# Performance work log

Measured on AMD Instinct MI355X. Metric: run time of the kernel, lower is better.

The kernel has to match this reference:

```python
import jax, jax.numpy as jnp
import numpy as np

EPS = 1e-5  # torch nn.LayerNorm default

def _ln(x, g, b):
    # LayerNorm over last dim with per-position affine params g, b (broadcastable)
    m = jnp.mean(x, axis=-1, keepdims=True)
    v = jnp.mean((x - m) ** 2, axis=-1, keepdims=True)
    return (x - m) * jax.lax.rsqrt(v + EPS) * g + b

def _mlp_ln(s, W1, b1, W2, b2, g, b):
    # Linear -> SiLU -> Linear -> LayerNorm
    h = jax.nn.silu(s @ W1 + b1) @ W2 + b2
    return _ln(h, g, b)

def setup_inputs() -> dict:
    key = jax.random.key(0)
    B, S, D = 4, 2048, 1024
    MEM, NOI, RES = 512, 64, 32
    ks = jax.random.split(key, 40)
    ki = iter(range(40))
    def nrm(shape, scale=0.02):
        return (jax.random.normal(ks[next(ki)], shape, jnp.float32) * scale)
    def gamma(shape):
        return jnp.ones(shape, jnp.float32) + nrm(shape)
    inp = {
        'x': jax.random.normal(ks[next(ki)], (B, S, D), jnp.float32),
        'pathway_ids': jax.random.randint(ks[next(ki)], (B, S), 0, 1000),
        'compartment_ids': jax.random.randint(ks[next(ki)], (B, S), 0, 5),
        'time_steps': jax.random.randint(ks[next(ki)], (B, S), 0, 5),
        'scale_type': jax.random.randint(ks[next(ki)], (B, S), 0, 3),
        'memory_state': jax.random.normal(ks[next(ki)], (B, MEM), jnp.float32),
        'noise_state': jax.random.normal(ks[next(ki)], (B, NOI), jnp.float32),
        'resource_state': jax.random.normal(ks[next(ki)], (B, RES), jnp.float32),
        # per-pathway / compartment / time / scale LayerNorm affine tables
        'pw_g': gamma((1000, D)), 'pw_b': nrm((1000, D)),
        'cp_g': gamma((5, D)), 'cp_b': nrm((5, D)),
        'tm_g': gamma((5, D)), 'tm_b': nrm((5, D)),
        'ms_g': gamma((3, D)), 'ms_b': nrm((3, D)),
        # memory / stochastic / resource MLP+LN stacks
        'mem_W1': nrm((MEM, D)), 'mem_b1': jnp.zeros((D,)), 'mem_W2': nrm((D, D)), 'mem_b2': jnp.zeros((D,)), 'mem_g': gamma((D,)), 'mem_be': jnp.zeros((D,)),
        'noi_W1': nrm((NOI, D)), 'noi_b1': jnp.zeros((D,)), 'noi_W2': nrm((D, D)), 'noi_b2': jnp.zeros((D,)), 'noi_g': gamma((D,)), 'noi_be': jnp.zeros((D,)),
        'res_W1': nrm((RES, D)), 'res_b1': jnp.zeros((D,)), 'res_W2': nrm((D, D)), 'res_b2': jnp.zeros((D,)), 'res_g': gamma((D,)), 'res_be': jnp.zeros((D,)),
        # integration MLP+LN
        'int_W1': nrm((6 * D, D)), 'int_b1': jnp.zeros((D,)), 'int_W2': nrm((D, D)), 'int_b2': jnp.zeros((D,)), 'int_g': gamma((D,)), 'int_be': jnp.zeros((D,)),
        'aw': jnp.ones((6,), jnp.float32) / 6.0,
    }
    return inp

def reference(x, pathway_ids, compartment_ids, time_steps, scale_type,
              memory_state, noise_state, resource_state,
              pw_g, pw_b, cp_g, cp_b, tm_g, tm_b, ms_g, ms_b,
              mem_W1, mem_b1, mem_W2, mem_b2, mem_g, mem_be,
              noi_W1, noi_b1, noi_W2, noi_b2, noi_g, noi_be,
              res_W1, res_b1, res_W2, res_b2, res_g, res_be,
              int_W1, int_b1, int_W2, int_b2, int_g, int_be, aw):
    # hierarchical: pathway-indexed LN, then compartment-indexed LN on its output
    h = _ln(x, pw_g[pathway_ids], pw_b[pathway_ids])
    h = _ln(h, cp_g[compartment_ids], cp_b[compartment_ids])
    # temporal: time-step-indexed LN of x
    t = _ln(x, tm_g[time_steps], tm_b[time_steps])
    # state-conditioned additive effects, broadcast over seq
    m = x + _mlp_ln(memory_state, mem_W1, mem_b1, mem_W2, mem_b2, mem_g, mem_be)[:, None, :]
    n = x + _mlp_ln(noise_state, noi_W1, noi_b1, noi_W2, noi_b2, noi_g, noi_be)[:, None, :]
    r = x + _mlp_ln(resource_state, res_W1, res_b1, res_W2, res_b2, res_g, res_be)[:, None, :]
    # multiscale: scale-indexed LN (scale in {0,1,2})
    s = _ln(x, ms_g[scale_type], ms_b[scale_type])
    w = jax.nn.softmax(aw)
    cat = jnp.concatenate([w[0] * h, w[1] * t, w[2] * m, w[3] * n, w[4] * r, w[5] * s], axis=-1)
    return _mlp_ln(cat, int_W1, int_b1, int_W2, int_b2, int_g, int_be)
```

## Files before the change

### kernel.cpp

```cpp
#include <hip/hip_runtime.h>
#include <cstdint>
#include <cstddef>

#define EPS_LN 1e-5f

typedef short bf16x8 __attribute__((ext_vector_type(8)));
typedef float f32x4 __attribute__((ext_vector_type(4)));
typedef unsigned int u32_gl __attribute__((address_space(1)));
typedef unsigned int u32_ld __attribute__((address_space(3)));

__device__ __forceinline__ unsigned short f2bf(float f) {
  union { float f; unsigned u; } v; v.f = f;
  unsigned r = v.u + 0x7fffu + ((v.u >> 16) & 1u);
  return (unsigned short)(r >> 16);
}

__device__ __forceinline__ void softmax6(const float* __restrict__ aw, float* w) {
  float m = aw[0];
  for (int i = 1; i < 6; ++i) m = fmaxf(m, aw[i]);
  float s = 0.f;
  for (int i = 0; i < 6; ++i) { w[i] = __expf(aw[i] - m); s += w[i]; }
  const float inv = 1.f / s;
  for (int i = 0; i < 6; ++i) w[i] *= inv;
}

__device__ __forceinline__ float block_sum256(float v, float* red) {
  for (int m = 32; m > 0; m >>= 1) v += __shfl_xor(v, m, 64);
  const int lane = threadIdx.x & 63, w = threadIdx.x >> 6;
  if (lane == 0) red[w] = v;
  __syncthreads();
  float r = red[0] + red[1] + red[2] + red[3];
  __syncthreads();
  return r;
}

__global__ __launch_bounds__(256) void state_h1_acc(
    const float* __restrict__ mem, const float* __restrict__ noi, const float* __restrict__ res,
    const float* __restrict__ mW1, const float* __restrict__ nW1, const float* __restrict__ rW1,
    const float* __restrict__ mb1, const float* __restrict__ nb1, const float* __restrict__ rb1,
    float* __restrict__ H1pre) {
  const int chunk = blockIdx.x, ks = blockIdx.y;
  const int j = chunk * 128 + (threadIdx.x & 127);
  const int half = threadIdx.x >> 7;
  int st, k0, klen, sstride;
  const float* W1; const float* sp; const float* b1;
  if (ks < 8)       { st = 0; W1 = mW1; sp = mem; b1 = mb1; sstride = 512; k0 = ks * 64 + half * 32; klen = 32; }
  else if (ks == 8) { st = 1; W1 = nW1; sp = noi; b1 = nb1; sstride = 64;  k0 = half * 32;           klen = 32; }
  else              { st = 2; W1 = rW1; sp = res; b1 = rb1; sstride = 32;  k0 = half * 16;           klen = 16; }
  float a0 = 0.f, a1 = 0.f, a2 = 0.f, a3 = 0.f;
  const float* wp = W1 + (size_t)k0 * 1024 + j;
  for (int it = 0; it < klen; ++it) {
    const float wv = wp[(size_t)it * 1024];
    const int k = k0 + it;
    a0 += sp[k] * wv;
    a1 += sp[sstride + k] * wv;
    a2 += sp[2 * sstride + k] * wv;
    a3 += sp[3 * sstride + k] * wv;
  }
  __shared__ float part[4][128];
  const int jl = threadIdx.x & 127;
  if (half) { part[0][jl] = a0; part[1][jl] = a1; part[2][jl] = a2; part[3][jl] = a3; }
  __syncthreads();
  if (!half) {
    const float bv = (ks == 0 || ks >= 8) ? b1[j] : 0.f;
    atomicAdd(&H1pre[(size_t)(st * 4 + 0) * 1024 + j], a0 + part[0][jl] + bv);
    atomicAdd(&H1pre[(size_t)(st * 4 + 1) * 1024 + j], a1 + part[1][jl] + bv);
    atomicAdd(&H1pre[(size_t)(st * 4 + 2) * 1024 + j], a2 + part[2][jl] + bv);
    atomicAdd(&H1pre[(size_t)(st * 4 + 3) * 1024 + j], a3 + part[3][jl] + bv);
  }
}

__global__ __launch_bounds__(256) void state_y_acc(
    const float* __restrict__ H1pre,
    const float* __restrict__ mW2, const float* __restrict__ nW2, const float* __restrict__ rW2,
    const float* __restrict__ mb2, const float* __restrict__ nb2, const float* __restrict__ rb2,
    float* __restrict__ Ys) {
  const int chunk = blockIdx.x, ks = blockIdx.y, st = blockIdx.z;
  const float* W2 = st == 0 ? mW2 : st == 1 ? nW2 : rW2;
  const float* b2 = st == 0 ? mb2 : st == 1 ? nb2 : rb2;
  const int j = chunk * 128 + (threadIdx.x & 127);
  const int half = threadIdx.x >> 7;
  const int k0 = ks * 64 + half * 32;
  const float* h1 = H1pre + (size_t)st * 4096;
  float a0 = 0.f, a1 = 0.f, a2 = 0.f, a3 = 0.f;
  const float* wp = W2 + (size_t)k0 * 1024 + j;
  for (int it = 0; it < 32; ++it) {
    const float wv = wp[(size_t)it * 1024];
    const int k = k0 + it;
    float h;
    h = h1[k];        a0 += (h / (1.f + __expf(-h))) * wv;
    h = h1[1024 + k]; a1 += (h / (1.f + __expf(-h))) * wv;
    h = h1[2048 + k]; a2 += (h / (1.f + __expf(-h))) * wv;
    h = h1[3072 + k]; a3 += (h / (1.f + __expf(-h))) * wv;
  }
  __shared__ float part[4][128];
  const int jl = threadIdx.x & 127;
  if (half) { part[0][jl] = a0; part[1][jl] = a1; part[2][jl] = a2; part[3][jl] = a3; }
  __syncthreads();
  if (!half) {
    const float bv = (ks == 0) ? b2[j] : 0.f;
    atomicAdd(&Ys[(size_t)(st * 4 + 0) * 1024 + j], a0 + part[0][jl] + bv);
    atomicAdd(&Ys[(size_t)(st * 4 + 1) * 1024 + j], a1 + part[1][jl] + bv);
    atomicAdd(&Ys[(size_t)(st * 4 + 2) * 1024 + j], a2 + part[2][jl] + bv);
    atomicAdd(&Ys[(size_t)(st * 4 + 3) * 1024 + j], a3 + part[3][jl] + bv);
  }
}

__global__ __launch_bounds__(256) void state_ln(
    const float* __restrict__ Ys,
    const float* __restrict__ mg, const float* __restrict__ mbe,
    const float* __restrict__ ng, const float* __restrict__ nbe,
    const float* __restrict__ rg, const float* __restrict__ rbe,
    const float* __restrict__ aw, float* __restrict__ mnrv) {
  __shared__ float red[4];
  const int st = blockIdx.x >> 2, b = blockIdx.x & 3;
  const float* g  = st == 0 ? mg  : st == 1 ? ng  : rg;
  const float* be = st == 0 ? mbe : st == 1 ? nbe : rbe;
  const float* y = Ys + (size_t)blockIdx.x * 1024;
  const int j = threadIdx.x * 4;
  float4 yv4 = *(const float4*)(y + j);
  float yv[4] = { yv4.x, yv4.y, yv4.z, yv4.w };
  float s = yv[0] + yv[1] + yv[2] + yv[3];
  float ss = yv[0]*yv[0] + yv[1]*yv[1] + yv[2]*yv[2] + yv[3]*yv[3];
  s = block_sum256(s, red);
  ss = block_sum256(ss, red);
  const float mu = s * (1.f / 1024.f);
  const float rstd = rsqrtf(ss * (1.f / 1024.f) - mu * mu + EPS_LN);
  float4 g4 = *(const float4*)(g + j);
  float4 b4 = *(const float4*)(be + j);
  float w[6];
  softmax6(aw, w);
  const float sc = w[2 + st];
  float* out = mnrv + (size_t)b * 3072 + st * 1024;
  out[j]     = ((yv[0] - mu) * rstd * g4.x + b4.x) * sc;
  out[j + 1] = ((yv[1] - mu) * rstd * g4.y + b4.y) * sc;
  out[j + 2] = ((yv[2] - mu) * rstd * g4.z + b4.z) * sc;
  out[j + 3] = ((yv[3] - mu) * rstd * g4.w + b4.w) * sc;
}

__global__ __launch_bounds__(256) void bias1_kernel(
    const float* __restrict__ mnrv, const float* __restrict__ iW1,
    const float* __restrict__ ib1, float* __restrict__ bias1) {
  const int chunk = blockIdx.x, ks = blockIdx.y;
  const int j = chunk * 128 + (threadIdx.x & 127);
  const int half = threadIdx.x >> 7;
  const int g0 = ks * 64 + half * 32;
  float acc0 = 0.f, acc1 = 0.f, acc2 = 0.f, acc3 = 0.f;
  const float* wp = iW1 + (size_t)(2048 + g0) * 1024 + j;
  for (int it = 0; it < 32; ++it) {
    const int g = g0 + it;
    const float wv = wp[(size_t)it * 1024];
    acc0 += mnrv[g] * wv;
    acc1 += mnrv[3072 + g] * wv;
    acc2 += mnrv[6144 + g] * wv;
    acc3 += mnrv[9216 + g] * wv;
  }
  __shared__ float part[4][128];
  const int jl = threadIdx.x & 127;
  if (half) { part[0][jl] = acc0; part[1][jl] = acc1; part[2][jl] = acc2; part[3][jl] = acc3; }
  __syncthreads();
  if (!half) {
    const float bv = (ks == 0) ? ib1[j] : 0.f;
    atomicAdd(&bias1[j],        acc0 + part[0][jl] + bv);
    atomicAdd(&bias1[1024 + j], acc1 + part[1][jl] + bv);
    atomicAdd(&bias1[2048 + j], acc2 + part[2][jl] + bv);
    atomicAdd(&bias1[3072 + j], acc3 + part[3][jl] + bv);
  }
}

__global__ __launch_bounds__(256) void prep_all(
    const float* __restrict__ x,
    const int* __restrict__ pid_, const int* __restrict__ cid_,
    const int* __restrict__ tid_, const int* __restrict__ sid_,
    const float* __restrict__ pwg, const float* __restrict__ pwb,
    const float* __restrict__ cpg, const float* __restrict__ cpb,
    const float* __restrict__ tmg, const float* __restrict__ tmb,
    const float* __restrict__ msg, const float* __restrict__ msb,
    const float* __restrict__ iW1, const float* __restrict__ iW2,
    const float* __restrict__ aw,
    unsigned short* __restrict__ cat4,
    unsigned short* __restrict__ W1T, unsigned short* __restrict__ W2T) {
  __shared__ float red[4];
  __shared__ float tile[32][33];
  int bi = blockIdx.x;
  if (bi < 8192) {
    const int row = bi;
    const int j = threadIdx.x * 4;
    float4 xv4 = *(const float4*)(x + (size_t)row * 1024 + j);
    float xv[4] = { xv4.x, xv4.y, xv4.z, xv4.w };
    float s = xv[0] + xv[1] + xv[2] + xv[3];
    float ss = xv[0]*xv[0] + xv[1]*xv[1] + xv[2]*xv[2] + xv[3]*xv[3];
    s = block_sum256(s, red);
    ss = block_sum256(ss, red);
    const float mu = s * (1.f / 1024.f);
    const float rstd = rsqrtf(ss * (1.f / 1024.f) - mu * mu + EPS_LN);
    float xh[4];
    for (int q = 0; q < 4; ++q) xh[q] = (xv[q] - mu) * rstd;
    const int pid = pid_[row], cid = cid_[row], tmi = tid_[row], msi = sid_[row];
    unsigned short* crow = cat4 + (size_t)row * 4096;

    float4 g4 = *(const float4*)(pwg + (size_t)pid * 1024 + j);
    float4 b4 = *(const float4*)(pwb + (size_t)pid * 1024 + j);
    float h1[4];
    h1[0] = xh[0] * g4.x + b4.x; h1[1] = xh[1] * g4.y + b4.y;
    h1[2] = xh[2] * g4.z + b4.z; h1[3] = xh[3] * g4.w + b4.w;
    float s1 = h1[0] + h1[1] + h1[2] + h1[3];
    float ss1 = h1[0]*h1[0] + h1[1]*h1[1] + h1[2]*h1[2] + h1[3]*h1[3];
    s1 = block_sum256(s1, red);
    ss1 = block_sum256(ss1, red);
    const float mu1 = s1 * (1.f / 1024.f);
    const float rstd1 = rsqrtf(ss1 * (1.f / 1024.f) - mu1 * mu1 + EPS_LN);
    g4 = *(const float4*)(cpg + (size_t)cid * 1024 + j);
    b4 = *(const float4*)(cpb + (size_t)cid * 1024 + j);
    ushort4 o;
    o.x = f2bf((h1[0] - mu1) * rstd1 * g4.x + b4.x);
    o.y = f2bf((h1[1] - mu1) * rstd1 * g4.y + b4.y);
    o.z = f2bf((h1[2] - mu1) * rstd1 * g4.z + b4.z);
    o.w = f2bf((h1[3] - mu1) * rstd1 * g4.w + b4.w);
    *(ushort4*)(crow + j) = o;

    g4 = *(const float4*)(tmg + (size_t)tmi * 1024 + j);
    b4 = *(const float4*)(tmb + (size_t)tmi * 1024 + j);
    o.x = f2bf(xh[0] * g4.x + b4.x); o.y = f2bf(xh[1] * g4.y + b4.y);
    o.z = f2bf(xh[2] * g4.z + b4.z); o.w = f2bf(xh[3] * g4.w + b4.w);
    *(ushort4*)(crow + 1024 + j) = o;

    o.x = f2bf(xv[0]); o.y = f2bf(xv[1]); o.z = f2bf(xv[2]); o.w = f2bf(xv[3]);
    *(ushort4*)(crow + 2048 + j) = o;

    g4 = *(const float4*)(msg + (size_t)msi * 1024 + j);
    b4 = *(const float4*)(msb + (size_t)msi * 1024 + j);
    o.x = f2bf(xh[0] * g4.x + b4.x); o.y = f2bf(xh[1] * g4.y + b4.y);
    o.z = f2bf(xh[2] * g4.z + b4.z); o.w = f2bf(xh[3] * g4.w + b4.w);
    *(ushort4*)(crow + 3072 + j) = o;
    return;
  }
  bi -= 8192;
  float w[6];
  softmax6(aw, w);
  const int r = threadIdx.x >> 3;
  const int c = (threadIdx.x & 7) * 4;
  if (bi < 4096) {
    const int k0 = (bi & 127) * 32, n0 = (bi >> 7) * 32;
    const int kk = k0 + r;
    float v[4];
    if (kk < 2048) {
      const float s = (kk < 1024) ? w[0] : w[1];
      float4 a = *(const float4*)(iW1 + (size_t)kk * 1024 + n0 + c);
      v[0] = s * a.x; v[1] = s * a.y; v[2] = s * a.z; v[3] = s * a.w;
    } else if (kk < 3072) {
      const float s2 = w[2], s3 = w[3], s4 = w[4];
      float4 a = *(const float4*)(iW1 + (size_t)kk * 1024 + n0 + c);
      float4 bq = *(const float4*)(iW1 + (size_t)(kk + 1024) * 1024 + n0 + c);
      float4 cq = *(const float4*)(iW1 + (size_t)(kk + 2048) * 1024 + n0 + c);
      v[0] = s2 * a.x + s3 * bq.x + s4 * cq.x;
      v[1] = s2 * a.y + s3 * bq.y + s4 * cq.y;
      v[2] = s2 * a.z + s3 * bq.z + s4 * cq.z;
      v[3] = s2 * a.w + s3 * bq.w + s4 * cq.w;
    } else {
      const float s = w[5];
      float4 a = *(const float4*)(iW1 + (size_t)(kk + 2048) * 1024 + n0 + c);
      v[0] = s * a.x; v[1] = s * a.y; v[2] = s * a.z; v[3] = s * a.w;
    }
    tile[r][c] = v[0]; tile[r][c + 1] = v[1]; tile[r][c + 2] = v[2]; tile[r][c + 3] = v[3];
    __syncthreads();
    const int nl = threadIdx.x >> 3;
    const int k4 = (threadIdx.x & 7) * 4;
    ushort4 o;
    o.x = f2bf(tile[k4][nl]);     o.y = f2bf(tile[k4 + 1][nl]);
    o.z = f2bf(tile[k4 + 2][nl]); o.w = f2bf(tile[k4 + 3][nl]);
    *(ushort4*)(W1T + (size_t)(n0 + nl) * 4096 + k0 + k4) = o;
    return;
  }
  bi -= 4096;
  {
    const int k0 = (bi & 31) * 32, n0 = (bi >> 5) * 32;
    float4 a = *(const float4*)(iW2 + (size_t)(k0 + r) * 1024 + n0 + c);
    tile[r][c] = a.x; tile[r][c + 1] = a.y; tile[r][c + 2] = a.z; tile[r][c + 3] = a.w;
    __syncthreads();
    const int nl = threadIdx.x >> 3, k4 = (threadIdx.x & 7) * 4;
    ushort4 o;
    o.x = f2bf(tile[k4][nl]);     o.y = f2bf(tile[k4 + 1][nl]);
    o.z = f2bf(tile[k4 + 2][nl]); o.w = f2bf(tile[k4 + 3][nl]);
    *(ushort4*)(W2T + (size_t)(n0 + nl) * 1024 + k0 + k4) = o;
  }
}

template <int EPI>
__global__ __launch_bounds__(256, 2) void gemm_bt(
    const unsigned short* __restrict__ A, const unsigned short* __restrict__ BT,
    const float* __restrict__ bias, void* __restrict__ out, int K) {
  __shared__ unsigned short At[2][128 * 32];
  __shared__ unsigned short Bt[2][128 * 32];
  const int t = threadIdx.x;
  const int lane = t & 63;
  const int wave = t >> 6;
  const int wr = wave >> 1, wc = wave & 1;
  const int quad = lane >> 4, l16 = lane & 15;
  const int bm = blockIdx.x, bn = blockIdx.y;
  const unsigned short* Ab = A + (size_t)bm * 128 * K;
  const unsigned short* Bb = BT + (size_t)bn * 128 * K;
  const int r0 = t >> 2, c0 = (t & 3) * 8;
  f32x4 acc[4][4];
#pragma unroll
  for (int i = 0; i < 4; ++i)
#pragma unroll
    for (int jj = 0; jj < 4; ++jj) { f32x4 z = {0.f, 0.f, 0.f, 0.f}; acc[i][jj] = z; }

  for (int kt = 0; kt < K; kt += 64) {
#pragma unroll
    for (int h = 0; h < 2; ++h) {
      const int ko = kt + h * 32;
      __builtin_amdgcn_global_load_lds(
          (const u32_gl*)(Ab + (size_t)r0 * K + ko + c0),
          (u32_ld*)(At[h] + t * 8), 16, 0, 0);
      __builtin_amdgcn_global_load_lds(
          (const u32_gl*)(Ab + (size_t)(r0 + 64) * K + ko + c0),
          (u32_ld*)(At[h] + (256 + t) * 8), 16, 0, 0);
      __builtin_amdgcn_global_load_lds(
          (const u32_gl*)(Bb + (size_t)r0 * K + ko + c0),
          (u32_ld*)(Bt[h] + t * 8), 16, 0, 0);
      __builtin_amdgcn_global_load_lds(
          (const u32_gl*)(Bb + (size_t)(r0 + 64) * K + ko + c0),
          (u32_ld*)(Bt[h] + (256 + t) * 8), 16, 0, 0);
    }
    __syncthreads();
#pragma unroll
    for (int h = 0; h < 2; ++h) {
      bf16x8 aF[4], bF[4];
#pragma unroll
      for (int mi = 0; mi < 4; ++mi)
        aF[mi] = *(const bf16x8*)(At[h] + (wr * 64 + mi * 16 + l16) * 32 + quad * 8);
#pragma unroll
      for (int ni = 0; ni < 4; ++ni)
        bF[ni] = *(const bf16x8*)(Bt[h] + (wc * 64 + ni * 16 + l16) * 32 + quad * 8);
#pragma unroll
      for (int mi = 0; mi < 4; ++mi)
#pragma unroll
        for (int ni = 0; ni < 4; ++ni)
          acc[mi][ni] = __builtin_amdgcn_mfma_f32_16x16x32_bf16(aF[mi], bF[ni], acc[mi][ni], 0, 0, 0);
    }
    __syncthreads();
  }
#pragma unroll
  for (int mi = 0; mi < 4; ++mi) {
#pragma unroll
    for (int ni = 0; ni < 4; ++ni) {
      const int col = bn * 128 + wc * 64 + ni * 16 + l16;
#pragma unroll
      for (int r = 0; r < 4; ++r) {
        const int row = bm * 128 + wr * 64 + mi * 16 + quad * 4 + r;
        float v = acc[mi][ni][r];
        if (EPI == 1) {
          v += bias[(size_t)(row >> 11) * 1024 + col];
          v = v / (1.f + __expf(-v));
          ((unsigned short*)out)[(size_t)row * 1024 + col] = f2bf(v);
        } else {
          v += bias[col];
          ((float*)out)[(size_t)row * 1024 + col] = v;
        }
      }
    }
  }
}

__global__ __launch_bounds__(256) void final_ln(
    const float* __restrict__ Y, const float* __restrict__ g,
    const float* __restrict__ be, float* __restrict__ out) {
  __shared__ float red[4];
  const int row = blockIdx.x;
  const int j = threadIdx.x * 4;
  float4 yv4 = *(const float4*)(Y + (size_t)row * 1024 + j);
  float yv[4] = { yv4.x, yv4.y, yv4.z, yv4.w };
  float s = yv[0] + yv[1] + yv[2] + yv[3];
  float ss = yv[0]*yv[0] + yv[1]*yv[1] + yv[2]*yv[2] + yv[3]*yv[3];
  s = block_sum256(s, red);
  ss = block_sum256(ss, red);
  const float mu = s * (1.f / 1024.f);
  const float rstd = rsqrtf(ss * (1.f / 1024.f) - mu * mu + EPS_LN);
  float4 g4 = *(const float4*)(g + j);
  float4 b4 = *(const float4*)(be + j);
  float4 o;
  o.x = (yv[0] - mu) * rstd * g4.x + b4.x;
  o.y = (yv[1] - mu) * rstd * g4.y + b4.y;
  o.z = (yv[2] - mu) * rstd * g4.z + b4.z;
  o.w = (yv[3] - mu) * rstd * g4.w + b4.w;
  *(float4*)(out + (size_t)row * 1024 + j) = o;
}

extern "C" void kernel_launch(void* const* d_in, const int* in_sizes, int n_in,
                              void* d_out, int out_size, void* d_ws, size_t ws_size,
                              hipStream_t stream) {
  const float* x   = (const float*)d_in[0];
  const int*   pid = (const int*)d_in[1];
  const int*   cid = (const int*)d_in[2];
  const int*   tms = (const int*)d_in[3];
  const int*   sct = (const int*)d_in[4];
  const float* mem = (const float*)d_in[5];
  const float* noi = (const float*)d_in[6];
  const float* res = (const float*)d_in[7];
  const float* pwg = (const float*)d_in[8];
  const float* pwb = (const float*)d_in[9];
  const float* cpg = (const float*)d_in[10];
  const float* cpb = (const float*)d_in[11];
  const float* tmg = (const float*)d_in[12];
  const float* tmb = (const float*)d_in[13];
  const float* msg = (const float*)d_in[14];
  const float* msb = (const float*)d_in[15];
  const float* mW1 = (const float*)d_in[16]; const float* mb1 = (const float*)d_in[17];
  const float* mW2 = (const float*)d_in[18]; const float* mb2 = (const float*)d_in[19];
  const float* mg  = (const float*)d_in[20]; const float* mbe = (const float*)d_in[21];
  const float* nW1 = (const float*)d_in[22]; const float* nb1 = (const float*)d_in[23];
  const float* nW2 = (const float*)d_in[24]; const float* nb2 = (const float*)d_in[25];
  const float* ng  = (const float*)d_in[26]; const float* nbe = (const float*)d_in[27];
  const float* rW1 = (const float*)d_in[28]; const float* rb1 = (const float*)d_in[29];
  const float* rW2 = (const float*)d_in[30]; const float* rb2 = (const float*)d_in[31];
  const float* rg  = (const float*)d_in[32]; const float* rbe = (const float*)d_in[33];
  const float* iW1 = (const float*)d_in[34]; const float* ib1 = (const float*)d_in[35];
  const float* iW2 = (const float*)d_in[36]; const float* ib2 = (const float*)d_in[37];
  const float* ig  = (const float*)d_in[38]; const float* ibe = (const float*)d_in[39];
  const float* aw  = (const float*)d_in[40];

  char* ws = (char*)d_ws;
  float* H1pre = (float*)ws;
  float* Ys    = H1pre + 12288;
  float* bias1 = Ys + 12288;
  float* mnrv  = bias1 + 4096;
  unsigned short* W1T  = (unsigned short*)(ws + (1ull << 20));
  unsigned short* W2T  = (unsigned short*)(ws + (9ull << 20));
  unsigned short* cat4 = (unsigned short*)(ws + (11ull << 20));
  unsigned short* Hb   = (unsigned short*)(ws + (75ull << 20));
  float* Ybuf          = (float*)cat4;

  hipMemsetAsync(ws, 0, (12288 + 12288 + 4096) * sizeof(float), stream);
  state_h1_acc<<<dim3(8, 10), 256, 0, stream>>>(mem, noi, res, mW1, nW1, rW1,
                                                mb1, nb1, rb1, H1pre);
  state_y_acc<<<dim3(8, 16, 3), 256, 0, stream>>>(H1pre, mW2, nW2, rW2,
                                                  mb2, nb2, rb2, Ys);
  state_ln<<<12, 256, 0, stream>>>(Ys, mg, mbe, ng, nbe, rg, rbe, aw, mnrv);
  bias1_kernel<<<dim3(8, 48), 256, 0, stream>>>(mnrv, iW1, ib1, bias1);
  prep_all<<<8192 + 4096 + 1024, 256, 0, stream>>>(
      x, pid, cid, tms, sct, pwg, pwb, cpg, cpb, tmg, tmb, msg, msb,
      iW1, iW2, aw, cat4, W1T, W2T);
  gemm_bt<1><<<dim3(64, 8), 256, 0, stream>>>(cat4, W1T, bias1, (void*)Hb, 4096);
  gemm_bt<2><<<dim3(64, 8), 256, 0, stream>>>(Hb, W2T, ib2, (void*)Ybuf, 1024);
  final_ln<<<8192, 256, 0, stream>>>(Ybuf, ig, ibe, (float*)d_out);
}
```

Baseline: 371.5 us.

## Fuse bias1 into prep kernel, deepen GEMM k-step, store GEMM2 output as bf16

Moves the bias1 reduction into extra blocks of the prep_all launch to drop a kernel launch. Doubles the GEMM k-tile per barrier from 64 to 128 using four shared buffers, cutting sync count at the cost of more LDS per block. Writes the second GEMM's output in bf16 and has final LayerNorm read bf16, halving intermediate memory traffic but adding rounding before normalization.

```diff
diff --git a/kernel.cpp b/kernel.cpp
--- a/kernel.cpp
+++ b/kernel.cpp
@@ -13,6 +13,11 @@
   union { float f; unsigned u; } v; v.f = f;
   unsigned r = v.u + 0x7fffu + ((v.u >> 16) & 1u);
   return (unsigned short)(r >> 16);
+}
+
+__device__ __forceinline__ float bf2f(unsigned short b) {
+  union { unsigned u; float f; } v; v.u = ((unsigned)b) << 16;
+  return v.f;
 }
 
 __device__ __forceinline__ void softmax6(const float* __restrict__ aw, float* w) {
@@ -138,36 +143,6 @@
   out[j + 3] = ((yv[3] - mu) * rstd * g4.w + b4.w) * sc;
 }
 
-__global__ __launch_bounds__(256) void bias1_kernel(
-    const float* __restrict__ mnrv, const float* __restrict__ iW1,
-    const float* __restrict__ ib1, float* __restrict__ bias1) {
-  const int chunk = blockIdx.x, ks = blockIdx.y;
-  const int j = chunk * 128 + (threadIdx.x & 127);
-  const int half = threadIdx.x >> 7;
-  const int g0 = ks * 64 + half * 32;
-  float acc0 = 0.f, acc1 = 0.f, acc2 = 0.f, acc3 = 0.f;
-  const float* wp = iW1 + (size_t)(2048 + g0) * 1024 + j;
-  for (int it = 0; it < 32; ++it) {
-    const int g = g0 + it;
-    const float wv = wp[(size_t)it * 1024];
-    acc0 += mnrv[g] * wv;
-    acc1 += mnrv[3072 + g] * wv;
-    acc2 += mnrv[6144 + g] * wv;
-    acc3 += mnrv[9216 + g] * wv;
-  }
-  __shared__ float part[4][128];
-  const int jl = threadIdx.x & 127;
-  if (half) { part[0][jl] = acc0; part[1][jl] = acc1; part[2][jl] = acc2; part[3][jl] = acc3; }
-  __syncthreads();
-  if (!half) {
-    const float bv = (ks == 0) ? ib1[j] : 0.f;
-    atomicAdd(&bias1[j],        acc0 + part[0][jl] + bv);
-    atomicAdd(&bias1[1024 + j], acc1 + part[1][jl] + bv);
-    atomicAdd(&bias1[2048 + j], acc2 + part[2][jl] + bv);
-    atomicAdd(&bias1[3072 + j], acc3 + part[3][jl] + bv);
-  }
-}
-
 __global__ __launch_bounds__(256) void prep_all(
     const float* __restrict__ x,
     const int* __restrict__ pid_, const int* __restrict__ cid_,
@@ -177,11 +152,14 @@
     const float* __restrict__ tmg, const float* __restrict__ tmb,
     const float* __restrict__ msg, const float* __restrict__ msb,
     const float* __restrict__ iW1, const float* __restrict__ iW2,
-    const float* __restrict__ aw,
+    const float* __restrict__ aw, const float* __restrict__ mnrv,
+    const float* __restrict__ ib1,
     unsigned short* __restrict__ cat4,
-    unsigned short* __restrict__ W1T, unsigned short* __restrict__ W2T) {
+    unsigned short* __restrict__ W1T, unsigned short* __restrict__ W2T,
+    float* __restrict__ bias1) {
   __shared__ float red[4];
   __shared__ float tile[32][33];
+  __shared__ float part[4][128];
   int bi = blockIdx.x;
   if (bi < 8192) {
     const int row = bi;
@@ -236,11 +214,11 @@
     return;
   }
   bi -= 8192;
-  float w[6];
-  softmax6(aw, w);
-  const int r = threadIdx.x >> 3;
-  const int c = (threadIdx.x & 7) * 4;
   if (bi < 4096) {
+    float w[6];
+    softmax6(aw, w);
+    const int r = threadIdx.x >> 3;
+    const int c = (threadIdx.x & 7) * 4;
     const int k0 = (bi & 127) * 32, n0 = (bi >> 7) * 32;
     const int kk = k0 + r;
     float v[4];
@@ -273,7 +251,9 @@
     return;
   }
   bi -= 4096;
-  {
+  if (bi < 1024) {
+    const int r = threadIdx.x >> 3;
+    const int c = (threadIdx.x & 7) * 4;
     const int k0 = (bi & 31) * 32, n0 = (bi >> 5) * 32;
     float4 a = *(const float4*)(iW2 + (size_t)(k0 + r) * 1024 + n0 + c);
     tile[r][c] = a.x; tile[r][c + 1] = a.y; tile[r][c + 2] = a.z; tile[r][c + 3] = a.w;
@@ -283,6 +263,34 @@
     o.x = f2bf(tile[k4][nl]);     o.y = f2bf(tile[k4 + 1][nl]);
     o.z = f2bf(tile[k4 + 2][nl]); o.w = f2bf(tile[k4 + 3][nl]);
     *(ushort4*)(W2T + (size_t)(n0 + nl) * 1024 + k0 + k4) = o;
+    return;
+  }
+  bi -= 1024;
+  {
+    const int chunk = bi & 7, ks = bi >> 3;
+    const int j = chunk * 128 + (threadIdx.x & 127);
+    const int half = threadIdx.x >> 7;
+    const int g0 = ks * 64 + half * 32;
+    float acc0 = 0.f, acc1 = 0.f, acc2 = 0.f, acc3 = 0.f;
+    const float* wp = iW1 + (size_t)(2048 + g0) * 1024 + j;
+    for (int it = 0; it < 32; ++it) {
+      const int g = g0 + it;
+      const float wv = wp[(size_t)it * 1024];
+      acc0 += mnrv[g] * wv;
+      acc1 += mnrv[3072 + g] * wv;
+      acc2 += mnrv[6144 + g] * wv;
+      acc3 += mnrv[9216 + g] * wv;
+    }
+    const int jl = threadIdx.x & 127;
+    if (half) { part[0][jl] = acc0; part[1][jl] = acc1; part[2][jl] = acc2; part[3][jl] = acc3; }
+    __syncthreads();
+    if (!half) {
+      const float bv = (ks == 0) ? ib1[j] : 0.f;
+      atomicAdd(&bias1[j],        acc0 + part[0][jl] + bv);
+      atomicAdd(&bias1[1024 + j], acc1 + part[1][jl] + bv);
+      atomicAdd(&bias1[2048 + j], acc2 + part[2][jl] + bv);
+      atomicAdd(&bias1[3072 + j], acc3 + part[3][jl] + bv);
+    }
   }
 }
 
@@ -290,8 +298,8 @@
 __global__ __launch_bounds__(256, 2) void gemm_bt(
     const unsigned short* __restrict__ A, const unsigned short* __restrict__ BT,
     const float* __restrict__ bias, void* __restrict__ out, int K) {
-  __shared__ unsigned short At[2][128 * 32];
-  __shared__ unsigned short Bt[2][128 * 32];
+  __shared__ unsigned short At[4][128 * 32];
+  __shared__ unsigned short Bt[4][128 * 32];
   const int t = threadIdx.x;
   const int lane = t & 63;
   const int wave = t >> 6;
@@ -307,9 +315,9 @@
 #pragma unroll
     for (int jj = 0; jj < 4; ++jj) { f32x4 z = {0.f, 0.f, 0.f, 0.f}; acc[i][jj] = z; }
 
-  for (int kt = 0; kt < K; kt += 64) {
-#pragma unroll
-    for (int h = 0; h < 2; ++h) {
+  for (int kt = 0; kt < K; kt += 128) {
+#pragma unroll
+    for (int h = 0; h < 4; ++h) {
       const int ko = kt + h * 32;
       __builtin_amdgcn_global_load_lds(
           (const u32_gl*)(Ab + (size_t)r0 * K + ko + c0),
@@ -326,7 +334,7 @@
     }
     __syncthreads();
 #pragma unroll
-    for (int h = 0; h < 2; ++h) {
+    for (int h = 0; h < 4; ++h) {
       bf16x8 aF[4], bF[4];
 #pragma unroll
       for (int mi = 0; mi < 4; ++mi)
@@ -357,7 +365,7 @@
           ((unsigned short*)out)[(size_t)row * 1024 + col] = f2bf(v);
         } else {
           v += bias[col];
-          ((float*)out)[(size_t)row * 1024 + col] = v;
+          ((unsigned short*)out)[(size_t)row * 1024 + col] = f2bf(v);
         }
       }
     }
@@ -365,13 +373,13 @@
 }
 
 __global__ __launch_bounds__(256) void final_ln(
-    const float* __restrict__ Y, const float* __restrict__ g,
+    const unsigned short* __restrict__ Y, const float* __restrict__ g,
     const float* __restrict__ be, float* __restrict__ out) {
   __shared__ float red[4];
   const int row = blockIdx.x;
   const int j = threadIdx.x * 4;
-  float4 yv4 = *(const float4*)(Y + (size_t)row * 1024 + j);
-  float yv[4] = { yv4.x, yv4.y, yv4.z, yv4.w };
+  ushort4 u = *(const ushort4*)(Y + (size_t)row * 1024 + j);
+  float yv[4] = { bf2f(u.x), bf2f(u.y), bf2f(u.z), bf2f(u.w) };
   float s = yv[0] + yv[1] + yv[2] + yv[3];
   float ss = yv[0]*yv[0] + yv[1]*yv[1] + yv[2]*yv[2] + yv[3]*yv[3];
   s = block_sum256(s, red);
@@ -430,7 +438,7 @@
   unsigned short* W2T  = (unsigned short*)(ws + (9ull << 20));
   unsigned short* cat4 = (unsigned short*)(ws + (11ull << 20));
   unsigned short* Hb   = (unsigned short*)(ws + (75ull << 20));
-  float* Ybuf          = (float*)cat4;
+  unsigned short* Yb   = cat4;
 
   hipMemsetAsync(ws, 0, (12288 + 12288 + 4096) * sizeof(float), stream);
   state_h1_acc<<<dim3(8, 10), 256, 0, stream>>>(mem, noi, res, mW1, nW1, rW1,
@@ -438,11 +446,10 @@
   state_y_acc<<<dim3(8, 16, 3), 256, 0, stream>>>(H1pre, mW2, nW2, rW2,
                                                   mb2, nb2, rb2, Ys);
   state_ln<<<12, 256, 0, stream>>>(Ys, mg, mbe, ng, nbe, rg, rbe, aw, mnrv);
-  bias1_kernel<<<dim3(8, 48), 256, 0, stream>>>(mnrv, iW1, ib1, bias1);
-  prep_all<<<8192 + 4096 + 1024, 256, 0, stream>>>(
+  prep_all<<<8192 + 4096 + 1024 + 384, 256, 0, stream>>>(
       x, pid, cid, tms, sct, pwg, pwb, cpg, cpb, tmg, tmb, msg, msb,
-      iW1, iW2, aw, cat4, W1T, W2T);
+      iW1, iW2, aw, mnrv, ib1, cat4, W1T, W2T, bias1);
   gemm_bt<1><<<dim3(64, 8), 256, 0, stream>>>(cat4, W1T, bias1, (void*)Hb, 4096);
-  gemm_bt<2><<<dim3(64, 8), 256, 0, stream>>>(Hb, W2T, ib2, (void*)Ybuf, 1024);
-  final_ln<<<8192, 256, 0, stream>>>(Ybuf, ig, ibe, (float*)d_out);
-}
+  gemm_bt<2><<<dim3(64, 8), 256, 0, stream>>>(Hb, W2T, ib2, (void*)Yb, 1024);
+  final_ln<<<8192, 256, 0, stream>>>(Yb, ig, ibe, (float*)d_out);
+}
```

Measured after the change: 364.5 us. About the same (-1.9%).
